# Kernel tuning notes

Hardware: AMD Instinct MI355X
Metric: run time of the kernel (lower is better)

The kernel has to match this reference:

```python
import jax, jax.numpy as jnp
import numpy as np

K = 16  # knn_graph k, loop=True (self included since d(i,i)=0 is minimal)


def _knn_idx(pos, k):
    # exact kNN via pairwise squared distances; [N, k] neighbor indices
    sq = jnp.sum(pos * pos, axis=-1)
    d2 = sq[:, None] + sq[None, :] - 2.0 * (pos @ pos.T)  # [N, N]
    _, idx = jax.lax.top_k(-d2, k)
    return idx


def _pointnet_conv(x, pos, idx, Wa, ba, Wb, bb):
    # PointNetConv: msg = MLP(concat(x_j, pos_j - pos_i)), max-aggregate over neighbors
    rel = pos[idx] - pos[:, None, :]                    # [N, K, 3]
    m = jnp.concatenate([x[idx], rel], axis=-1)          # [N, K, Cin+3]
    h = jax.nn.relu(m @ Wa + ba) @ Wb + bb               # [N, K, Cout]
    return jnp.max(h, axis=1)                            # [N, Cout]


def setup_inputs() -> dict:
    key = jax.random.key(0)
    ks = jax.random.split(key, 13)
    N = 8192
    c1, c2, c3 = 64, 64, 128
    s = lambda fi: 1.0 / np.sqrt(fi)
    pos = jax.random.normal(ks[0], (N, 3), dtype=jnp.float32)
    return {
        "pos": pos,
        "W1a": jax.random.normal(ks[1], (3 + 3, c1), jnp.float32) * s(6),
        "b1a": jnp.zeros((c1,), jnp.float32),
        "W1b": jax.random.normal(ks[2], (c1, c1), jnp.float32) * s(c1),
        "b1b": jnp.zeros((c1,), jnp.float32),
        "W2a": jax.random.normal(ks[3], (c1 + 3, c2), jnp.float32) * s(c1 + 3),
        "b2a": jnp.zeros((c2,), jnp.float32),
        "W2b": jax.random.normal(ks[4], (c2, c2), jnp.float32) * s(c2),
        "b2b": jnp.zeros((c2,), jnp.float32),
        "W3a": jax.random.normal(ks[5], (c2 + 3, c3), jnp.float32) * s(c2 + 3),
        "b3a": jnp.zeros((c3,), jnp.float32),
        "W3b": jax.random.normal(ks[6], (c3, c3), jnp.float32) * s(c3),
        "b3b": jnp.zeros((c3,), jnp.float32),
    }


def reference(pos, W1a, b1a, W1b, b1b, W2a, b2a, W2b, b2b, W3a, b3a, W3b, b3b):
    idx = _knn_idx(pos, K)
    h1 = jax.nn.relu(_pointnet_conv(pos, pos, idx, W1a, b1a, W1b, b1b))
    h2 = jax.nn.relu(_pointnet_conv(h1, pos, idx, W2a, b2a, W2b, b2b))
    h3 = jax.nn.relu(_pointnet_conv(h2, pos, idx, W3a, b3a, W3b, b3b))
    return (h1, h2, h3)
```

## Files before the change

### kernel.cpp

```cpp
#include <hip/hip_runtime.h>
#include <math.h>

#define N_PTS 8192
#define KNN 16

typedef __attribute__((ext_vector_type(8))) short bf16x8;
typedef __attribute__((ext_vector_type(4))) float f32x4v;

__device__ __forceinline__ unsigned short f2bf(float f)
{
    unsigned u = __float_as_uint(f);
    u = u + 0x7fffu + ((u >> 16) & 1u);
    return (unsigned short)(u >> 16);
}
__device__ __forceinline__ unsigned pack2(float a, float b)
{
    return (unsigned)f2bf(a) | ((unsigned)f2bf(b) << 16);
}
__device__ __forceinline__ float bf2f(unsigned short h)
{
    return __uint_as_float((unsigned)h << 16);
}
__device__ __forceinline__ float rfl(float x)
{
    return __int_as_float(__builtin_amdgcn_readfirstlane(__float_as_int(x)));
}

__global__ __launch_bounds__(256) void prep_all(
    const float* __restrict__ pos, float4* __restrict__ pos4,
    unsigned short* __restrict__ v1,
    const float* __restrict__ w1a, const float* __restrict__ b1a,
    const float* __restrict__ w1b, const float* __restrict__ w2b,
    const float* __restrict__ w3b,
    uint4* __restrict__ dst)
{
    const int b = blockIdx.x;
    if (b < 48) {
        if (threadIdx.x >= 64) return;
        const float* Ws[3] = {w1b, w2b, w3b};
        const int Kd[3] = {64, 64, 128};
        const int Nd[3] = {64, 64, 128};
        const int start[4] = {0, 8, 16, 48};
        int m = 0;
        while (b >= start[m + 1]) ++m;
        const int f  = b - start[m];
        const int NT = Nd[m] / 16;
        const int ks = f / NT, nt = f % NT;
        const int lane = threadIdx.x;
        const int c  = nt * 16 + (lane & 15);
        const int k0 = ks * 32 + (lane >> 4) * 8;
        const int N = Nd[m];
        const float* W = Ws[m];
        float v[8];
#pragma unroll
        for (int j = 0; j < 8; ++j) v[j] = W[(k0 + j) * N + c];
        uint4 o;
        o.x = pack2(v[0], v[1]); o.y = pack2(v[2], v[3]);
        o.z = pack2(v[4], v[5]); o.w = pack2(v[6], v[7]);
        dst[b * 64 + lane] = o;
    } else if (b < 80) {
        const int i = (b - 48) * 256 + threadIdx.x;
        const float x = pos[i * 3 + 0];
        const float y = pos[i * 3 + 1];
        const float z = pos[i * 3 + 2];
        pos4[i] = make_float4(x, y, z, fmaf(x, x, fmaf(y, y, z * z)));
    } else {
        const int i = (b - 80) * 256 + threadIdx.x;
        const float px = pos[i * 3 + 0], py = pos[i * 3 + 1], pz = pos[i * 3 + 2];
#pragma unroll
        for (int c8 = 0; c8 < 64; c8 += 8) {
            unsigned o[4];
#pragma unroll
            for (int d2 = 0; d2 < 4; ++d2) {
                float r[2];
#pragma unroll
                for (int e = 0; e < 2; ++e) {
                    const int c = c8 + d2 * 2 + e;
                    float acc = b1a[c];
                    acc = fmaf(px, w1a[0 * 64 + c] + w1a[3 * 64 + c], acc);
                    acc = fmaf(py, w1a[1 * 64 + c] + w1a[4 * 64 + c], acc);
                    acc = fmaf(pz, w1a[2 * 64 + c] + w1a[5 * 64 + c], acc);
                    r[e] = acc;
                }
                o[d2] = pack2(r[0], r[1]);
            }
            *reinterpret_cast<uint4*>(v1 + i * 64 + c8) = make_uint4(o[0], o[1], o[2], o[3]);
        }
    }
}

__device__ __forceinline__ unsigned sortkey(const float d2)
{
    unsigned u = __float_as_uint(d2);
    u ^= (unsigned)((int)u >> 31) | 0x80000000u;
    return u;
}
__device__ __forceinline__ float unkey(unsigned k)
{
    const unsigned u = (k & 0x80000000u) ? (k ^ 0x80000000u) : ~k;
    return __uint_as_float(u);
}

constexpr int CAP   = 128;
constexpr int QB    = 16;
constexpr int TILE  = 1024;
constexpr int NTL   = N_PTS / TILE;

__device__ __forceinline__ void stage_tile(const float4* src, float4* dst)
{
    __builtin_amdgcn_global_load_lds(
        (const __attribute__((address_space(1))) void*)src,
        (__attribute__((address_space(3))) void*)dst, 16, 0, 0);
}

__global__ __launch_bounds__(512) void knn_kernel(const float4* __restrict__ pos4,
                                                  int* __restrict__ idx_out)
{
    __shared__ float4 tile[2][TILE];
    __shared__ unsigned minkey[QB][64];
    __shared__ float Ts[QB];
    __shared__ unsigned long long surv[QB][CAP];
    __shared__ int scnt[QB];

    const int tid   = threadIdx.x;
    const int w     = tid >> 6;
    const int lane  = tid & 63;
    const int qbase = blockIdx.x * QB;

    if (tid < QB) scnt[tid] = 0;
    reinterpret_cast<unsigned*>(minkey)[tid]       = 0xFFFFFFFFu;
    reinterpret_cast<unsigned*>(minkey)[tid + 512] = 0xFFFFFFFFu;

    float qx[QB], qy[QB], qz[QB];
#pragma unroll
    for (int qi = 0; qi < QB; ++qi) {
        const float4 qp = pos4[qbase + qi];
        qx[qi] = rfl(-2.0f * qp.x);
        qy[qi] = rfl(-2.0f * qp.y);
        qz[qi] = rfl(-2.0f * qp.z);
    }

    const float4* src = pos4 + w * 128 + lane;
    float4* dst0 = &tile[0][w * 128];
    float4* dst1 = &tile[1][w * 128];

    float mn[QB];
#pragma unroll
    for (int qi = 0; qi < QB; ++qi) mn[qi] = 1e30f;

    stage_tile(src,      dst0);
    stage_tile(src + 64, dst0 + 64);
    __syncthreads();
#pragma unroll 1
    for (int t = 0; t < NTL - 1; ++t) {
        float4* nd = (t & 1) ? dst0 : dst1;
        stage_tile(src + (t + 1) * TILE,      nd);
        stage_tile(src + (t + 1) * TILE + 64, nd + 64);
        asm volatile("s_waitcnt vmcnt(2)" ::: "memory");
        __builtin_amdgcn_sched_barrier(0);
        const float4 p0 = tile[t & 1][w * 128 + lane];
        const float4 p1 = tile[t & 1][w * 128 + 64 + lane];
#pragma unroll
        for (int qi = 0; qi < QB; ++qi) {
            const float s0 = fmaf(qx[qi], p0.x, fmaf(qy[qi], p0.y, fmaf(qz[qi], p0.z, p0.w)));
            const float s1 = fmaf(qx[qi], p1.x, fmaf(qy[qi], p1.y, fmaf(qz[qi], p1.z, p1.w)));
            mn[qi] = fminf(mn[qi], fminf(s0, s1));
        }
    }
    {
        asm volatile("s_waitcnt vmcnt(0)" ::: "memory");
        __builtin_amdgcn_sched_barrier(0);
        const int t = NTL - 1;
        const float4 p0 = tile[t & 1][w * 128 + lane];
        const float4 p1 = tile[t & 1][w * 128 + 64 + lane];
#pragma unroll
        for (int qi = 0; qi < QB; ++qi) {
            const float s0 = fmaf(qx[qi], p0.x, fmaf(qy[qi], p0.y, fmaf(qz[qi], p0.z, p0.w)));
            const float s1 = fmaf(qx[qi], p1.x, fmaf(qy[qi], p1.y, fmaf(qz[qi], p1.z, p1.w)));
            mn[qi] = fminf(mn[qi], fminf(s0, s1));
        }
    }
#pragma unroll
    for (int qi = 0; qi < QB; ++qi) atomicMin(&minkey[qi][lane], sortkey(mn[qi]));
    __syncthreads();

#pragma unroll
    for (int k = 0; k < 2; ++k) {
        const int q = w * 2 + k;
        unsigned v = minkey[q][lane];
#pragma unroll
        for (int kk = 2; kk <= 64; kk <<= 1)
#pragma unroll
            for (int j = kk >> 1; j > 0; j >>= 1) {
                const unsigned o = __shfl_xor(v, j);
                const bool up = ((lane & kk) == 0);
                const bool lo = ((lane & j) == 0);
                v = (up == lo) ? min(v, o) : max(v, o);
            }
        if (lane == 15) Ts[q] = unkey(v);
    }
    __syncthreads();

    float T[QB];
#pragma unroll
    for (int qi = 0; qi < QB; ++qi) T[qi] = rfl(Ts[qi]);

    stage_tile(src,      dst0);
    stage_tile(src + 64, dst0 + 64);
#pragma unroll 1
    for (int t = 0; t < NTL - 1; ++t) {
        float4* nd = (t & 1) ? dst0 : dst1;
        stage_tile(src + (t + 1) * TILE,      nd);
        stage_tile(src + (t + 1) * TILE + 64, nd + 64);
        asm volatile("s_waitcnt vmcnt(2)" ::: "memory");
        __builtin_amdgcn_sched_barrier(0);
#pragma unroll
        for (int u = 0; u < 2; ++u) {
            const float4 p = tile[t & 1][w * 128 + u * 64 + lane];
            const int j = t * TILE + w * 128 + u * 64 + lane;
#pragma unroll
            for (int qi = 0; qi < QB; ++qi) {
                const float s = fmaf(qx[qi], p.x, fmaf(qy[qi], p.y, fmaf(qz[qi], p.z, p.w)));
                if (s <= T[qi]) {
                    const int slot = atomicAdd(&scnt[qi], 1);
                    if (slot < CAP)
                        surv[qi][slot] = ((unsigned long long)sortkey(s) << 32) | (unsigned)j;
                }
            }
        }
    }
    {
        asm volatile("s_waitcnt vmcnt(0)" ::: "memory");
        __builtin_amdgcn_sched_barrier(0);
        const int t = NTL - 1;
#pragma unroll
        for (int u = 0; u < 2; ++u) {
            const float4 p = tile[t & 1][w * 128 + u * 64 + lane];
            const int j = t * TILE + w * 128 + u * 64 + lane;
#pragma unroll
            for (int qi = 0; qi < QB; ++qi) {
                const float s = fmaf(qx[qi], p.x, fmaf(qy[qi], p.y, fmaf(qz[qi], p.z, p.w)));
                if (s <= T[qi]) {
                    const int slot = atomicAdd(&scnt[qi], 1);
                    if (slot < CAP)
                        surv[qi][slot] = ((unsigned long long)sortkey(s) << 32) | (unsigned)j;
                }
            }
        }
    }
    __syncthreads();

#pragma unroll
    for (int k = 0; k < 2; ++k) {
        const int q = w * 2 + k;
        const int n = min(scnt[q], CAP);
        const unsigned long long k0 = (lane < n) ? surv[q][lane] : ~0ull;
        const unsigned long long k1 = (lane + 64 < n) ? surv[q][lane + 64] : ~0ull;
        int r0 = 0, r1 = 0;
        for (int e = 0; e < n; ++e) {
            const unsigned long long ke = surv[q][e];
            r0 += (ke < k0) ? 1 : 0;
            r1 += (ke < k1) ? 1 : 0;
        }
        if (lane < n && r0 < KNN)
            idx_out[(qbase + q) * KNN + r0] = (int)(unsigned)(k0 & 0xFFFFFFFFu);
        if (lane + 64 < n && r1 < KNN)
            idx_out[(qbase + q) * KNN + r1] = (int)(unsigned)(k1 & 0xFFFFFFFFu);
    }
}

template <int CMID, int COUT, int WM, int WN, int VNEXT>
__global__ __launch_bounds__(256) void conv_fused(
    const unsigned short* __restrict__ v, const float* __restrict__ pos,
    const int* __restrict__ idx,
    const float* __restrict__ WaRel,
    const uint4* __restrict__ fB, const float* __restrict__ bb,
    const float* __restrict__ Wnext, const float* __restrict__ bnext,
    float* __restrict__ out, unsigned short* __restrict__ vout)
{
    constexpr int PB  = 8, M = 128;
    constexpr int KP2 = CMID + 8;
    constexpr int KS2 = CMID / 32;
    constexpr int NT  = COUT / 16;
    constexpr int NTW = NT / WN;
    constexpr int MFW = (M / 16) / WM;

    __shared__ int nbr[M];
    __shared__ float ubuf[PB][CMID];
    __shared__ __align__(16) unsigned short hbuf[M * KP2];

    const int tid  = threadIdx.x;
    const int lane = tid & 63;
    const int w    = tid >> 6;
    const int wm   = w / WN, wn = w % WN;
    const int i0   = blockIdx.x * PB;

    if (tid < M) nbr[tid] = idx[i0 * KNN + tid];
    for (int e = tid; e < PB * CMID; e += 256) {
        const int pt = e / CMID, c = e % CMID;
        float u = pos[(i0 + pt) * 3 + 0] * WaRel[c];
        u = fmaf(pos[(i0 + pt) * 3 + 1], WaRel[CMID + c], u);
        u = fmaf(pos[(i0 + pt) * 3 + 2], WaRel[2 * CMID + c], u);
        ubuf[pt][c] = u;
    }
    __syncthreads();

    {
        const int row = tid >> 1, hh = tid & 1;
        const int j = nbr[row], pt = row >> 4;
        const int cb = hh * (CMID / 2);
#pragma unroll
        for (int cc = 0; cc < CMID / 2; cc += 8) {
            const uint4 vv = *reinterpret_cast<const uint4*>(v + j * CMID + cb + cc);
            const unsigned dw[4] = {vv.x, vv.y, vv.z, vv.w};
            unsigned o[4];
#pragma unroll
            for (int d2 = 0; d2 < 4; ++d2) {
                const int c = cb + cc + d2 * 2;
                const float flo = __uint_as_float(dw[d2] << 16);
                const float fhi = __uint_as_float(dw[d2] & 0xffff0000u);
                const float rlo = fmaxf(flo - ubuf[pt][c],     0.0f);
                const float rhi = fmaxf(fhi - ubuf[pt][c + 1], 0.0f);
                o[d2] = pack2(rlo, rhi);
            }
            *reinterpret_cast<uint4*>(&hbuf[row * KP2 + cb + cc]) =
                make_uint4(o[0], o[1], o[2], o[3]);
        }
    }
    __syncthreads();

    float outv[MFW][NTW];
    {
        uint4 b2[KS2][NTW];
#pragma unroll
        for (int ks = 0; ks < KS2; ++ks)
#pragma unroll
            for (int nt = 0; nt < NTW; ++nt)
                b2[ks][nt] = fB[(ks * NT + wn * NTW + nt) * 64 + lane];

        f32x4v acc2[MFW][NTW];
#pragma unroll
        for (int mf = 0; mf < MFW; ++mf)
#pragma unroll
            for (int nt = 0; nt < NTW; ++nt) acc2[mf][nt] = (f32x4v)0.0f;

#pragma unroll
        for (int mf = 0; mf < MFW; ++mf) {
            bf16x8 a[KS2];
#pragma unroll
            for (int ks = 0; ks < KS2; ++ks)
                a[ks] = *reinterpret_cast<const bf16x8*>(
                    &hbuf[((wm * MFW + mf) * 16 + (lane & 15)) * KP2 + ks * 32 + (lane >> 4) * 8]);
#pragma unroll
            for (int nt = 0; nt < NTW; ++nt)
#pragma unroll
                for (int ks = 0; ks < KS2; ++ks)
                    acc2[mf][nt] = __builtin_amdgcn_mfma_f32_16x16x32_bf16(
                        a[ks], __builtin_bit_cast(bf16x8, b2[ks][nt]), acc2[mf][nt], 0, 0, 0);
        }

        float bbv[NTW];
#pragma unroll
        for (int nt = 0; nt < NTW; ++nt) bbv[nt] = bb[(wn * NTW + nt) * 16 + (lane & 15)];

#pragma unroll
        for (int mf = 0; mf < MFW; ++mf)
#pragma unroll
            for (int nt = 0; nt < NTW; ++nt) {
                const f32x4v t = acc2[mf][nt];
                float m0 = fmaxf(fmaxf(t[0], t[1]), fmaxf(t[2], t[3]));
                m0 = fmaxf(m0, __shfl_xor(m0, 16));
                m0 = fmaxf(m0, __shfl_xor(m0, 32));
                outv[mf][nt] = fmaxf(m0 + bbv[nt], 0.0f);
            }
    }
    __syncthreads();

#pragma unroll
    for (int mf = 0; mf < MFW; ++mf)
#pragma unroll
        for (int nt = 0; nt < NTW; ++nt) {
            if (lane < 16) {
                const int pt = wm * MFW + mf;
                const int c  = (wn * NTW + nt) * 16 + lane;
                out[(i0 + pt) * COUT + c] = outv[mf][nt];
                if constexpr (VNEXT > 0) hbuf[pt * KP2 + c] = f2bf(outv[mf][nt]);
            }
        }

    if constexpr (VNEXT > 0) {
        __syncthreads();
        constexpr int CPT = VNEXT / 32;
        const int pt = tid >> 5;
        const int c0 = (tid & 31) * CPT;
        float acc[CPT];
#pragma unroll
        for (int e = 0; e < CPT; ++e) acc[e] = bnext[c0 + e];
        for (int k = 0; k < COUT; ++k) {
            const float hk = bf2f(hbuf[pt * KP2 + k]);
#pragma unroll
            for (int e = 0; e < CPT; ++e)
                acc[e] = fmaf(hk, Wnext[k * VNEXT + c0 + e], acc[e]);
        }
#pragma unroll
        for (int d = 0; d < 3; ++d) {
            const float pd = pos[(i0 + pt) * 3 + d];
#pragma unroll
            for (int e = 0; e < CPT; ++e)
                acc[e] = fmaf(pd, Wnext[(COUT + d) * VNEXT + c0 + e], acc[e]);
        }
        if constexpr (CPT == 2) {
            *reinterpret_cast<unsigned*>(vout + (i0 + pt) * VNEXT + c0) = pack2(acc[0], acc[1]);
        } else {
            uint2 o;
            o.x = pack2(acc[0], acc[1]);
            o.y = pack2(acc[2], acc[3]);
            *reinterpret_cast<uint2*>(vout + (i0 + pt) * VNEXT + c0) = o;
        }
    }
}

extern "C" void kernel_launch(void* const* d_in, const int* in_sizes, int n_in,
                              void* d_out, int out_size, void* d_ws, size_t ws_size,
                              hipStream_t stream)
{
    const float* pos = (const float*)d_in[0];
    const float* W1a = (const float*)d_in[1];
    const float* b1a = (const float*)d_in[2];
    const float* W1b = (const float*)d_in[3];
    const float* b1b = (const float*)d_in[4];
    const float* W2a = (const float*)d_in[5];
    const float* b2a = (const float*)d_in[6];
    const float* W2b = (const float*)d_in[7];
    const float* b2b = (const float*)d_in[8];
    const float* W3a = (const float*)d_in[9];
    const float* b3a = (const float*)d_in[10];
    const float* W3b = (const float*)d_in[11];
    const float* b3b = (const float*)d_in[12];

    float* out = (float*)d_out;
    float* h1 = out;
    float* h2 = out + N_PTS * 64;
    float* h3 = out + N_PTS * 128;

    int*            idx     = (int*)d_ws;
    uint4*          wsFrags = (uint4*)((char*)d_ws + 524288);
    unsigned short* v3      = (unsigned short*)((char*)d_ws + 589824);

    float4*         pos4 = (float4*)h3;
    unsigned short* v1   = (unsigned short*)((char*)h3 + 131072);
    unsigned short* v2   = (unsigned short*)((char*)h3 + 1179648);

    prep_all<<<112, 256, 0, stream>>>(pos, pos4, v1, W1a, b1a, W1b, W2b, W3b, wsFrags);
    knn_kernel<<<N_PTS / QB, 512, 0, stream>>>(pos4, idx);

    const uint4* fW1b = wsFrags + 0 * 64;
    const uint4* fW2b = wsFrags + 8 * 64;
    const uint4* fW3b = wsFrags + 16 * 64;

    conv_fused<64, 64, 4, 1, 64><<<N_PTS / 8, 256, 0, stream>>>(
        v1, pos, idx, W1a + 3 * 64, fW1b, b1b, W2a, b2a, h1, v2);
    conv_fused<64, 64, 4, 1, 128><<<N_PTS / 8, 256, 0, stream>>>(
        v2, pos, idx, W2a + 64 * 64, fW2b, b2b, W3a, b3a, h2, v3);
    conv_fused<128, 128, 2, 2, 0><<<N_PTS / 8, 256, 0, stream>>>(
        v3, pos, idx, W3a + 64 * 128, fW3b, b3b, nullptr, nullptr, h3, nullptr);
}
```

Baseline: 81.54 us.

## Shrink kNN tiles and survivor buffer, add occupancy hint and early-out filter

The kNN kernel halves the staged position tile so each wave handles one float4 per tile instead of two, and cuts the survivor capacity per query from 128 to 96. Together these shrink LDS use, and a min-blocks launch-bounds hint asks for more resident blocks. The filter pass now computes all 16 query distances first and only enters the atomic-append path when any of them passes, so divergent branching stays off the common path. The rank loop is unrolled. The tighter register budget from the occupancy hint may cause spills with 16 queries held in registers, and the smaller capacity may drop survivors when many points tie near the threshold.

```diff
diff --git a/kernel.cpp b/kernel.cpp
--- a/kernel.cpp
+++ b/kernel.cpp
@@ -38,7 +38,6 @@
     if (b < 48) {
         if (threadIdx.x >= 64) return;
         const float* Ws[3] = {w1b, w2b, w3b};
-        const int Kd[3] = {64, 64, 128};
         const int Nd[3] = {64, 64, 128};
         const int start[4] = {0, 8, 16, 48};
         int m = 0;
@@ -101,9 +100,9 @@
     return __uint_as_float(u);
 }
 
-constexpr int CAP   = 128;
+constexpr int CAP   = 96;
 constexpr int QB    = 16;
-constexpr int TILE  = 1024;
+constexpr int TILE  = 512;
 constexpr int NTL   = N_PTS / TILE;
 
 __device__ __forceinline__ void stage_tile(const float4* src, float4* dst)
@@ -113,8 +112,8 @@
         (__attribute__((address_space(3))) void*)dst, 16, 0, 0);
 }
 
-__global__ __launch_bounds__(512) void knn_kernel(const float4* __restrict__ pos4,
-                                                  int* __restrict__ idx_out)
+__global__ __launch_bounds__(512, 8) void knn_kernel(const float4* __restrict__ pos4,
+                                                     int* __restrict__ idx_out)
 {
     __shared__ float4 tile[2][TILE];
     __shared__ unsigned minkey[QB][64];
@@ -140,44 +139,30 @@
         qz[qi] = rfl(-2.0f * qp.z);
     }
 
-    const float4* src = pos4 + w * 128 + lane;
-    float4* dst0 = &tile[0][w * 128];
-    float4* dst1 = &tile[1][w * 128];
+    const float4* src = pos4 + w * 64 + lane;
+    float4* dst0 = &tile[0][w * 64];
+    float4* dst1 = &tile[1][w * 64];
 
     float mn[QB];
 #pragma unroll
     for (int qi = 0; qi < QB; ++qi) mn[qi] = 1e30f;
 
-    stage_tile(src,      dst0);
-    stage_tile(src + 64, dst0 + 64);
+    stage_tile(src, dst0);
     __syncthreads();
 #pragma unroll 1
-    for (int t = 0; t < NTL - 1; ++t) {
-        float4* nd = (t & 1) ? dst0 : dst1;
-        stage_tile(src + (t + 1) * TILE,      nd);
-        stage_tile(src + (t + 1) * TILE + 64, nd + 64);
-        asm volatile("s_waitcnt vmcnt(2)" ::: "memory");
+    for (int t = 0; t < NTL; ++t) {
+        if (t + 1 < NTL) {
+            stage_tile(src + (t + 1) * TILE, (t & 1) ? dst0 : dst1);
+            asm volatile("s_waitcnt vmcnt(1)" ::: "memory");
+        } else {
+            asm volatile("s_waitcnt vmcnt(0)" ::: "memory");
+        }
         __builtin_amdgcn_sched_barrier(0);
-        const float4 p0 = tile[t & 1][w * 128 + lane];
-        const float4 p1 = tile[t & 1][w * 128 + 64 + lane];
+        const float4 p = tile[t & 1][w * 64 + lane];
 #pragma unroll
         for (int qi = 0; qi < QB; ++qi) {
-            const float s0 = fmaf(qx[qi], p0.x, fmaf(qy[qi], p0.y, fmaf(qz[qi], p0.z, p0.w)));
-            const float s1 = fmaf(qx[qi], p1.x, fmaf(qy[qi], p1.y, fmaf(qz[qi], p1.z, p1.w)));
-            mn[qi] = fminf(mn[qi], fminf(s0, s1));
-        }
-    }
-    {
-        asm volatile("s_waitcnt vmcnt(0)" ::: "memory");
-        __builtin_amdgcn_sched_barrier(0);
-        const int t = NTL - 1;
-        const float4 p0 = tile[t & 1][w * 128 + lane];
-        const float4 p1 = tile[t & 1][w * 128 + 64 + lane];
-#pragma unroll
-        for (int qi = 0; qi < QB; ++qi) {
-            const float s0 = fmaf(qx[qi], p0.x, fmaf(qy[qi], p0.y, fmaf(qz[qi], p0.z, p0.w)));
-            const float s1 = fmaf(qx[qi], p1.x, fmaf(qy[qi], p1.y, fmaf(qz[qi], p1.z, p1.w)));
-            mn[qi] = fminf(mn[qi], fminf(s0, s1));
+            const float s = fmaf(qx[qi], p.x, fmaf(qy[qi], p.y, fmaf(qz[qi], p.z, p.w)));
+            mn[qi] = fminf(mn[qi], s);
         }
     }
 #pragma unroll
@@ -205,47 +190,33 @@
 #pragma unroll
     for (int qi = 0; qi < QB; ++qi) T[qi] = rfl(Ts[qi]);
 
-    stage_tile(src,      dst0);
-    stage_tile(src + 64, dst0 + 64);
+    stage_tile(src, dst0);
 #pragma unroll 1
-    for (int t = 0; t < NTL - 1; ++t) {
-        float4* nd = (t & 1) ? dst0 : dst1;
-        stage_tile(src + (t + 1) * TILE,      nd);
-        stage_tile(src + (t + 1) * TILE + 64, nd + 64);
-        asm volatile("s_waitcnt vmcnt(2)" ::: "memory");
+    for (int t = 0; t < NTL; ++t) {
+        if (t + 1 < NTL) {
+            stage_tile(src + (t + 1) * TILE, (t & 1) ? dst0 : dst1);
+            asm volatile("s_waitcnt vmcnt(1)" ::: "memory");
+        } else {
+            asm volatile("s_waitcnt vmcnt(0)" ::: "memory");
+        }
         __builtin_amdgcn_sched_barrier(0);
-#pragma unroll
-        for (int u = 0; u < 2; ++u) {
-            const float4 p = tile[t & 1][w * 128 + u * 64 + lane];
-            const int j = t * TILE + w * 128 + u * 64 + lane;
-#pragma unroll
-            for (int qi = 0; qi < QB; ++qi) {
-                const float s = fmaf(qx[qi], p.x, fmaf(qy[qi], p.y, fmaf(qz[qi], p.z, p.w)));
-                if (s <= T[qi]) {
+        const float4 p = tile[t & 1][w * 64 + lane];
+        const int j = t * TILE + w * 64 + lane;
+        float s[QB];
+        bool hit = false;
+#pragma unroll
+        for (int qi = 0; qi < QB; ++qi) {
+            s[qi] = fmaf(qx[qi], p.x, fmaf(qy[qi], p.y, fmaf(qz[qi], p.z, p.w)));
+            hit = hit | (s[qi] <= T[qi]);
+        }
+        if (__builtin_expect(hit, 0)) {
+#pragma unroll
+            for (int qi = 0; qi < QB; ++qi)
+                if (s[qi] <= T[qi]) {
                     const int slot = atomicAdd(&scnt[qi], 1);
                     if (slot < CAP)
-                        surv[qi][slot] = ((unsigned long long)sortkey(s) << 32) | (unsigned)j;
+                        surv[qi][slot] = ((unsigned long long)sortkey(s[qi]) << 32) | (unsigned)j;
                 }
-            }
-        }
-    }
-    {
-        asm volatile("s_waitcnt vmcnt(0)" ::: "memory");
-        __builtin_amdgcn_sched_barrier(0);
-        const int t = NTL - 1;
-#pragma unroll
-        for (int u = 0; u < 2; ++u) {
-            const float4 p = tile[t & 1][w * 128 + u * 64 + lane];
-            const int j = t * TILE + w * 128 + u * 64 + lane;
-#pragma unroll
-            for (int qi = 0; qi < QB; ++qi) {
-                const float s = fmaf(qx[qi], p.x, fmaf(qy[qi], p.y, fmaf(qz[qi], p.z, p.w)));
-                if (s <= T[qi]) {
-                    const int slot = atomicAdd(&scnt[qi], 1);
-                    if (slot < CAP)
-                        surv[qi][slot] = ((unsigned long long)sortkey(s) << 32) | (unsigned)j;
-                }
-            }
         }
     }
     __syncthreads();
@@ -257,6 +228,7 @@
         const unsigned long long k0 = (lane < n) ? surv[q][lane] : ~0ull;
         const unsigned long long k1 = (lane + 64 < n) ? surv[q][lane + 64] : ~0ull;
         int r0 = 0, r1 = 0;
+#pragma unroll 4
         for (int e = 0; e < n; ++e) {
             const unsigned long long ke = surv[q][e];
             r0 += (ke < k0) ? 1 : 0;
```

Measured after the change: 144.8 us. 1.78x slower.
